# Optimization experiments

Hardware: AMD Instinct MI355X
Metric: run time of the kernel (lower is better)

## Reference

```python
import jax, jax.numpy as jnp
import numpy as np

ALIGN_SCALE = 3.0
UNIF_SCALE = 1.0
EPS = 1e-12  # torch F.normalize eps


def _normalize(x):
    n = jnp.linalg.norm(x, axis=-1, keepdims=True)
    return x / jnp.maximum(n, EPS)


def _unif_loss(a, b):
    # log(mean(exp(-2 * ||a_i - b_j||^2))) over all N*M pairs, fused via GEMM identity
    sq_a = jnp.sum(a * a, axis=1)  # [N]
    sq_b = jnp.sum(b * b, axis=1)  # [M]
    # squared distances: ||a||^2 + ||b||^2 - 2 a.b, clipped at 0 for numerics
    d2 = jnp.maximum(sq_a[:, None] + sq_b[None, :] - 2.0 * (a @ b.T), 0.0)  # [N, M]
    return jnp.log(jnp.mean(jnp.exp(-2.0 * d2)))


def setup_inputs() -> dict:
    key = jax.random.key(0)
    k1, k2 = jax.random.split(key)
    N, D = 8192, 512
    return {
        "image_embed": jax.random.normal(k1, (N, D), dtype=jnp.float32),
        "text_embed": jax.random.normal(k2, (N, D), dtype=jnp.float32),
    }


def reference(image_embed, text_embed):
    img = _normalize(image_embed)
    txt = _normalize(text_embed)
    # alignment: mean squared L2 between paired embeddings
    diff = img - txt
    align_loss = jnp.mean(jnp.sum(diff * diff, axis=1))
    # single device: gathered-all tensors equal the local tensors
    text_unif = _unif_loss(txt, txt)
    image_unif = _unif_loss(img, img)
    unif_loss = (text_unif + image_unif) / 2.0
    return ALIGN_SCALE * align_loss + UNIF_SCALE * unif_loss
```

## Files before the change

kernel.cpp:

```cpp
#include <hip/hip_runtime.h>
#include <hip/hip_bf16.h>


#define NROWS 8192
#define DBYTES 512
#define NT    64
#define NBLK  1056
#define SCALE_SPLAT 0x75757575

typedef __attribute__((ext_vector_type(8)))  int   int8v;
typedef __attribute__((ext_vector_type(4)))  int   int4v;
typedef __attribute__((ext_vector_type(16))) float float16v;

__device__ inline void load_lds16(const void* g, void* l) {
    __builtin_amdgcn_global_load_lds(
        (const __attribute__((address_space(1))) void*)g,
        (__attribute__((address_space(3))) void*)l, 16, 0, 0);
}

__device__ inline int swz(int r) { return (r ^ (r >> 3)) & 7; }

__global__ __launch_bounds__(256) void normalize_kernel(
    const float* __restrict__ img, const float* __restrict__ txt,
    unsigned char* __restrict__ nimg, unsigned char* __restrict__ ntxt,
    float* __restrict__ alignp,
    float* __restrict__ S)
{
    if (blockIdx.x == 0 && threadIdx.x < 64) S[threadIdx.x] = 0.0f;

    const int lane = threadIdx.x & 63;
    const int wave = threadIdx.x >> 6;
    const int row  = blockIdx.x * 4 + wave;

    const float4* pi = (const float4*)(img + (size_t)row * 512);
    const float4* pt = (const float4*)(txt + (size_t)row * 512);
    const float4 i0 = pi[lane], i1 = pi[lane + 64];
    const float4 t0 = pt[lane], t1 = pt[lane + 64];

    float ssi = i0.x*i0.x + i0.y*i0.y + i0.z*i0.z + i0.w*i0.w
              + i1.x*i1.x + i1.y*i1.y + i1.z*i1.z + i1.w*i1.w;
    float sst = t0.x*t0.x + t0.y*t0.y + t0.z*t0.z + t0.w*t0.w
              + t1.x*t1.x + t1.y*t1.y + t1.z*t1.z + t1.w*t1.w;
    float dot = i0.x*t0.x + i0.y*t0.y + i0.z*t0.z + i0.w*t0.w
              + i1.x*t1.x + i1.y*t1.y + i1.z*t1.z + i1.w*t1.w;

    #pragma unroll
    for (int off = 1; off < 64; off <<= 1) {
        ssi += __shfl_xor(ssi, off);
        sst += __shfl_xor(sst, off);
        dot += __shfl_xor(dot, off);
    }
    const float inv_i = 1.0f / fmaxf(sqrtf(ssi), 1e-12f);
    const float inv_t = 1.0f / fmaxf(sqrtf(sst), 1e-12f);
    const float si = 1024.0f * inv_i;
    const float st = 1024.0f * inv_t;

    int p0 = __builtin_amdgcn_cvt_pk_fp8_f32(i0.x*si, i0.y*si, 0, false);
    p0     = __builtin_amdgcn_cvt_pk_fp8_f32(i0.z*si, i0.w*si, p0, true);
    int p1 = __builtin_amdgcn_cvt_pk_fp8_f32(i1.x*si, i1.y*si, 0, false);
    p1     = __builtin_amdgcn_cvt_pk_fp8_f32(i1.z*si, i1.w*si, p1, true);
    int q0 = __builtin_amdgcn_cvt_pk_fp8_f32(t0.x*st, t0.y*st, 0, false);
    q0     = __builtin_amdgcn_cvt_pk_fp8_f32(t0.z*st, t0.w*st, q0, true);
    int q1 = __builtin_amdgcn_cvt_pk_fp8_f32(t1.x*st, t1.y*st, 0, false);
    q1     = __builtin_amdgcn_cvt_pk_fp8_f32(t1.z*st, t1.w*st, q1, true);

    int* oi = (int*)(nimg + (size_t)row * DBYTES);
    int* ot = (int*)(ntxt + (size_t)row * DBYTES);
    oi[lane] = p0; oi[lane + 64] = p1;
    ot[lane] = q0; ot[lane + 64] = q1;

    __shared__ float r4[4];
    if (lane == 0) r4[wave] = dot * inv_i * inv_t;
    __syncthreads();
    if (threadIdx.x == 0)
        alignp[blockIdx.x] = r4[0] + r4[1] + r4[2] + r4[3];
}

__global__ __launch_bounds__(256, 2) void gram_kernel(
    const unsigned char* __restrict__ A0,
    const unsigned char* __restrict__ A1,
    float* __restrict__ S)
{
    const int b = blockIdx.x;
    int I = (int)((65.0f - sqrtf(4225.0f - 4.0f * (float)b)) * 0.5f);
    while ((I + 1) * (64 - I) <= b) ++I;
    while (I * (65 - I) > b) --I;
    const int j = 2 * I + (b - I * (65 - I));

    const unsigned char* __restrict__ A = blockIdx.y ? A1 : A0;
    const int tid  = threadIdx.x;
    const int lane = tid & 63;
    const int wave = tid >> 6;
    const int wm = wave & 1, wn = wave >> 1;
    const int lr = lane & 31;
    const int h  = lane >> 5;

    const unsigned char* gA = A + (size_t)I * 256 * DBYTES;
    const unsigned char* gB = A + (size_t)j * 128 * DBYTES;

    __shared__ __align__(16) unsigned char ldsA[256 * 128];
    __shared__ __align__(16) unsigned char ldsB[128 * 128];

    float16v acc[4][2];
    #pragma unroll
    for (int a = 0; a < 4; ++a)
        #pragma unroll
        for (int c = 0; c < 2; ++c)
            #pragma unroll
            for (int r = 0; r < 16; ++r) acc[a][c][r] = 0.0f;

    for (int k0 = 0; k0 < DBYTES; k0 += 128) {
        #pragma unroll
        for (int rnd = 0; rnd < 8; ++rnd) {
            const int slot = rnd * 4096 + tid * 16;
            const int r    = slot >> 7;
            const int cp   = (slot >> 4) & 7;
            const int cl   = cp ^ swz(r);
            load_lds16(gA + (size_t)r * DBYTES + k0 + cl * 16, &ldsA[slot]);
        }
        #pragma unroll
        for (int rnd = 0; rnd < 4; ++rnd) {
            const int slot = rnd * 4096 + tid * 16;
            const int r    = slot >> 7;
            const int cp   = (slot >> 4) & 7;
            const int cl   = cp ^ swz(r);
            load_lds16(gB + (size_t)r * DBYTES + k0 + cl * 16, &ldsB[slot]);
        }
        __syncthreads();

        #pragma unroll
        for (int kk = 0; kk < 2; ++kk) {
            const int c0 = kk * 4 + h * 2;
            int8v av[4], bv[2];
            #pragma unroll
            for (int mt = 0; mt < 4; ++mt) {
                const int r = wm * 128 + mt * 32 + lr;
                const int s0 = swz(r);
                *((int4v*)&av[mt])     = *(const int4v*)&ldsA[r * 128 + ((c0    ) ^ s0) * 16];
                *((int4v*)&av[mt] + 1) = *(const int4v*)&ldsA[r * 128 + ((c0 + 1) ^ s0) * 16];
            }
            #pragma unroll
            for (int nt = 0; nt < 2; ++nt) {
                const int r = wn * 64 + nt * 32 + lr;
                const int s0 = swz(r);
                *((int4v*)&bv[nt])     = *(const int4v*)&ldsB[r * 128 + ((c0    ) ^ s0) * 16];
                *((int4v*)&bv[nt] + 1) = *(const int4v*)&ldsB[r * 128 + ((c0 + 1) ^ s0) * 16];
            }
            #pragma unroll
            for (int mt = 0; mt < 4; ++mt)
                #pragma unroll
                for (int nt = 0; nt < 2; ++nt)
                    acc[mt][nt] = __builtin_amdgcn_mfma_scale_f32_32x32x64_f8f6f4(
                        av[mt], bv[nt], acc[mt][nt],
                        0, 0,
                        0, SCALE_SPLAT,
                        0, SCALE_SPLAT);
        }
        __syncthreads();
    }

    const int r128 = 2 * I + wm;
    const float wv = (j > r128) ? 2.0f : ((j == r128) ? 1.0f : 0.0f);
    float s = 0.0f;
    #pragma unroll
    for (int mt = 0; mt < 4; ++mt)
        #pragma unroll
        for (int nt = 0; nt < 2; ++nt)
            #pragma unroll
            for (int r2 = 0; r2 < 16; ++r2) {
                const float g = acc[mt][nt][r2];
                s += __expf(4.0f * fminf(g, 1.0f) - 4.0f);
            }
    s *= wv;
    #pragma unroll
    for (int off = 32; off; off >>= 1) s += __shfl_down(s, off);
    __shared__ float ps[4];
    if (lane == 0) ps[wave] = s;
    __syncthreads();
    if (tid == 0) {
        const float tot = ps[0] + ps[1] + ps[2] + ps[3];
        atomicAdd(&S[blockIdx.y * 32 + (blockIdx.x & 31)], tot);
    }
}

__global__ __launch_bounds__(256) void finalize_kernel(
    const float* __restrict__ S,
    const float* __restrict__ alignp,
    float* __restrict__ out)
{
    const int tid = threadIdx.x;
    float a = 0.0f;
    #pragma unroll
    for (int k = 0; k < 8; ++k) a += alignp[tid + 256 * k];
    #pragma unroll
    for (int off = 32; off; off >>= 1) a += __shfl_down(a, off);
    __shared__ float r4[4];
    if ((tid & 63) == 0) r4[tid >> 6] = a;
    __syncthreads();
    if (tid == 0) {
        const double A = (double)r4[0] + r4[1] + r4[2] + r4[3];
        double si = 0.0, st = 0.0;
        for (int k = 0; k < 32; ++k) { si += S[k]; st += S[32 + k]; }
        const double align = 2.0 - 2.0 * A / (double)NROWS;
        const double n2 = (double)NROWS * (double)NROWS;
        const double unif = 0.5 * (log(si / n2) + log(st / n2));
        out[0] = (float)(3.0 * align + unif);
    }
}

extern "C" void kernel_launch(void* const* d_in, const int* in_sizes, int n_in,
                              void* d_out, int out_size, void* d_ws, size_t ws_size,
                              hipStream_t stream) {
    const float* img = (const float*)d_in[0];
    const float* txt = (const float*)d_in[1];
    char* ws = (char*)d_ws;
    unsigned char* nimg = (unsigned char*)ws;
    unsigned char* ntxt = (unsigned char*)(ws + (size_t)NROWS * DBYTES);
    float* S      = (float*)(ws + 2 * (size_t)NROWS * DBYTES);
    float* alignp = S + 64;

    normalize_kernel<<<NROWS / 4, 256, 0, stream>>>(img, txt, nimg, ntxt, alignp, S);
    dim3 grid(NBLK, 2);
    gram_kernel<<<grid, 256, 0, stream>>>(nimg, ntxt, S);
    finalize_kernel<<<1, 256, 0, stream>>>(S, alignp, (float*)d_out);
}
```

Baseline: 123.9 us.

## Use 256x256 symmetric tiles with double-buffered LDS staging in gram kernel

The gram kernel switches from 256x128 tiles over the upper triangle to square 256x256 tiles over the upper-triangular tile pairs, halving the block count and doubling per-wave MFMA work (4x4 accumulators). It also double-buffers LDS so the next K chunk loads while the current one is computed, removing one barrier per iteration. This is meant to improve operand reuse and hide load latency. In exchange it uses 128KB of LDS and more registers, limiting occupancy to one block per CU, and leaves fewer blocks to balance across CUs.

```diff
diff --git a/kernel.cpp b/kernel.cpp
--- a/kernel.cpp
+++ b/kernel.cpp
@@ -4,8 +4,8 @@
 
 #define NROWS 8192
 #define DBYTES 512
-#define NT    64
-#define NBLK  1056
+#define NP    32
+#define NBLK  528
 #define SCALE_SPLAT 0x75757575
 
 typedef __attribute__((ext_vector_type(8)))  int   int8v;
@@ -76,16 +76,16 @@
         alignp[blockIdx.x] = r4[0] + r4[1] + r4[2] + r4[3];
 }
 
-__global__ __launch_bounds__(256, 2) void gram_kernel(
+__global__ __launch_bounds__(256, 1) void gram_kernel(
     const unsigned char* __restrict__ A0,
     const unsigned char* __restrict__ A1,
     float* __restrict__ S)
 {
     const int b = blockIdx.x;
-    int I = (int)((65.0f - sqrtf(4225.0f - 4.0f * (float)b)) * 0.5f);
-    while ((I + 1) * (64 - I) <= b) ++I;
-    while (I * (65 - I) > b) --I;
-    const int j = 2 * I + (b - I * (65 - I));
+    int I = (int)((65.0f - sqrtf(4225.0f - 8.0f * (float)b)) * 0.5f);
+    while ((I + 1) * (64 - I) / 2 <= b) ++I;
+    while (I * (65 - I) / 2 > b) --I;
+    const int J = I + (b - I * (65 - I) / 2);
 
     const unsigned char* __restrict__ A = blockIdx.y ? A1 : A0;
     const int tid  = threadIdx.x;
@@ -96,76 +96,80 @@
     const int h  = lane >> 5;
 
     const unsigned char* gA = A + (size_t)I * 256 * DBYTES;
-    const unsigned char* gB = A + (size_t)j * 128 * DBYTES;
-
-    __shared__ __align__(16) unsigned char ldsA[256 * 128];
-    __shared__ __align__(16) unsigned char ldsB[128 * 128];
-
-    float16v acc[4][2];
+    const unsigned char* gB = A + (size_t)J * 256 * DBYTES;
+
+    __shared__ __align__(16) unsigned char ldsA[2][256 * 128];
+    __shared__ __align__(16) unsigned char ldsB[2][256 * 128];
+
+    #define STAGE(buf, kb)                                                     \
+        do {                                                                   \
+            _Pragma("unroll")                                                  \
+            for (int rnd = 0; rnd < 8; ++rnd) {                                \
+                const int slot = rnd * 4096 + tid * 16;                        \
+                const int r    = slot >> 7;                                    \
+                const int cp   = (slot >> 4) & 7;                              \
+                const int cl   = cp ^ swz(r);                                  \
+                load_lds16(gA + (size_t)r * DBYTES + (kb) + cl * 16,           \
+                           &ldsA[buf][slot]);                                  \
+                load_lds16(gB + (size_t)r * DBYTES + (kb) + cl * 16,           \
+                           &ldsB[buf][slot]);                                  \
+            }                                                                  \
+        } while (0)
+
+    float16v acc[4][4];
     #pragma unroll
     for (int a = 0; a < 4; ++a)
         #pragma unroll
-        for (int c = 0; c < 2; ++c)
+        for (int c = 0; c < 4; ++c)
             #pragma unroll
             for (int r = 0; r < 16; ++r) acc[a][c][r] = 0.0f;
 
-    for (int k0 = 0; k0 < DBYTES; k0 += 128) {
-        #pragma unroll
-        for (int rnd = 0; rnd < 8; ++rnd) {
-            const int slot = rnd * 4096 + tid * 16;
-            const int r    = slot >> 7;
-            const int cp   = (slot >> 4) & 7;
-            const int cl   = cp ^ swz(r);
-            load_lds16(gA + (size_t)r * DBYTES + k0 + cl * 16, &ldsA[slot]);
-        }
-        #pragma unroll
-        for (int rnd = 0; rnd < 4; ++rnd) {
-            const int slot = rnd * 4096 + tid * 16;
-            const int r    = slot >> 7;
-            const int cp   = (slot >> 4) & 7;
-            const int cl   = cp ^ swz(r);
-            load_lds16(gB + (size_t)r * DBYTES + k0 + cl * 16, &ldsB[slot]);
-        }
+    STAGE(0, 0);
+
+    #pragma unroll
+    for (int k0 = 0; k0 < 4; ++k0) {
+        const int buf = k0 & 1;
         __syncthreads();
+        if (k0 < 3) STAGE(buf ^ 1, (k0 + 1) * 128);
 
         #pragma unroll
         for (int kk = 0; kk < 2; ++kk) {
             const int c0 = kk * 4 + h * 2;
-            int8v av[4], bv[2];
+            int8v av[4], bv[4];
             #pragma unroll
             for (int mt = 0; mt < 4; ++mt) {
                 const int r = wm * 128 + mt * 32 + lr;
                 const int s0 = swz(r);
-                *((int4v*)&av[mt])     = *(const int4v*)&ldsA[r * 128 + ((c0    ) ^ s0) * 16];
-                *((int4v*)&av[mt] + 1) = *(const int4v*)&ldsA[r * 128 + ((c0 + 1) ^ s0) * 16];
+                *((int4v*)&av[mt])     = *(const int4v*)&ldsA[buf][r * 128 + ((c0    ) ^ s0) * 16];
+                *((int4v*)&av[mt] + 1) = *(const int4v*)&ldsA[buf][r * 128 + ((c0 + 1) ^ s0) * 16];
             }
             #pragma unroll
-            for (int nt = 0; nt < 2; ++nt) {
-                const int r = wn * 64 + nt * 32 + lr;
+            for (int nt = 0; nt < 4; ++nt) {
+                const int r = wn * 128 + nt * 32 + lr;
                 const int s0 = swz(r);
-                *((int4v*)&bv[nt])     = *(const int4v*)&ldsB[r * 128 + ((c0    ) ^ s0) * 16];
-                *((int4v*)&bv[nt] + 1) = *(const int4v*)&ldsB[r * 128 + ((c0 + 1) ^ s0) * 16];
+                *((int4v*)&bv[nt])     = *(const int4v*)&ldsB[buf][r * 128 + ((c0    ) ^ s0) * 16];
+                *((int4v*)&bv[nt] + 1) = *(const int4v*)&ldsB[buf][r * 128 + ((c0 + 1) ^ s0) * 16];
             }
             #pragma unroll
             for (int mt = 0; mt < 4; ++mt)
                 #pragma unroll
-                for (int nt = 0; nt < 2; ++nt)
+                for (int nt = 0; nt < 4; ++nt)
                     acc[mt][nt] = __builtin_amdgcn_mfma_scale_f32_32x32x64_f8f6f4(
                         av[mt], bv[nt], acc[mt][nt],
                         0, 0,
                         0, SCALE_SPLAT,
                         0, SCALE_SPLAT);
         }
-        __syncthreads();
     }
 
     const int r128 = 2 * I + wm;
-    const float wv = (j > r128) ? 2.0f : ((j == r128) ? 1.0f : 0.0f);
+    const int c128 = 2 * J + wn;
+    const float wv = (c128 > r128) ? 2.0f : ((c128 == r128) ? 1.0f : 0.0f);
     float s = 0.0f;
     #pragma unroll
     for (int mt = 0; mt < 4; ++mt)
         #pragma unroll
-        for (int nt = 0; nt < 2; ++nt)
+        for (int nt = 0; nt < 4; ++nt)
             #pragma unroll
             for (int r2 = 0; r2 < 16; ++r2) {
                 const float g = acc[mt][nt][r2];
@@ -181,6 +185,7 @@
         const float tot = ps[0] + ps[1] + ps[2] + ps[3];
         atomicAdd(&S[blockIdx.y * 32 + (blockIdx.x & 31)], tot);
     }
+    #undef STAGE
 }
 
 __global__ __launch_bounds__(256) void finalize_kernel(
```

After: 133.2 us. 7.5% more time.
